# Performance work log

Measured on AMD Instinct MI355X. Metric: run time of the kernel, lower is better.

## Reference

```python
import jax, jax.numpy as jnp
import numpy as np

N_NODES = 50000
N_EDGES = 800000
IN_CH = 128
HID = 32
HEADS = 4
LATENT = 64
NEG_SLOPE = 0.2  # PyG GATConv default


def setup_inputs() -> dict:
    key = jax.random.key(0)
    ks = jax.random.split(key, 12)
    HC = HID * HEADS
    inp = {
        "x": jax.random.normal(ks[0], (N_NODES, IN_CH), dtype=jnp.float32),
        "edge_index": jax.random.randint(ks[1], (2, N_EDGES), 0, N_NODES, dtype=jnp.int64),
        # GATConv params
        "W_gat": jax.random.normal(ks[2], (IN_CH, HC), dtype=jnp.float32) / np.sqrt(IN_CH),
        "b_gat": jnp.zeros((HC,), dtype=jnp.float32),
        "att_src": jax.random.normal(ks[3], (HEADS, HID), dtype=jnp.float32) / np.sqrt(HID),
        "att_dst": jax.random.normal(ks[4], (HEADS, HID), dtype=jnp.float32) / np.sqrt(HID),
        # encoder / decoder / output linears
        "W_enc": jax.random.normal(ks[5], (HC, LATENT), dtype=jnp.float32) / np.sqrt(HC),
        "b_enc": jnp.zeros((LATENT,), dtype=jnp.float32),
        "W_dec": jax.random.normal(ks[6], (LATENT, HC), dtype=jnp.float32) / np.sqrt(LATENT),
        "b_dec": jnp.zeros((HC,), dtype=jnp.float32),
        "W_out": jax.random.normal(ks[7], (HC, IN_CH), dtype=jnp.float32) / np.sqrt(HC),
        "b_out": jnp.zeros((IN_CH,), dtype=jnp.float32),
    }
    return inp


def reference(x, edge_index, W_gat, b_gat, att_src, att_dst,
              W_enc, b_enc, W_dec, b_dec, W_out, b_out):
    N = x.shape[0]
    H, C = att_src.shape
    # PyG GATConv adds self-loops by default
    loops = jnp.arange(N, dtype=edge_index.dtype)
    src = jnp.concatenate([edge_index[0], loops])  # message sources (x_j)
    dst = jnp.concatenate([edge_index[1], loops])  # aggregation targets (x_i)

    h = (x @ W_gat).reshape(N, H, C)               # [N,H,C]
    a_src = jnp.einsum('nhc,hc->nh', h, att_src)   # [N,H]
    a_dst = jnp.einsum('nhc,hc->nh', h, att_dst)   # [N,H]

    e = jax.nn.leaky_relu(a_src[src] + a_dst[dst], NEG_SLOPE)  # [E,H]
    # segment softmax over destination nodes (numerically stable)
    e_max = jax.ops.segment_max(e, dst, num_segments=N)
    e_exp = jnp.exp(e - e_max[dst])
    denom = jax.ops.segment_sum(e_exp, dst, num_segments=N)
    alpha = e_exp / (denom[dst] + 1e-16)           # [E,H]

    msg = h[src] * alpha[:, :, None]               # [E,H,C]
    agg = jax.ops.segment_sum(msg, dst, num_segments=N)  # [N,H,C]
    gat_out = agg.reshape(N, H * C) + b_gat        # concat heads + bias

    x1 = jax.nn.elu(gat_out)
    encoded = x1 @ W_enc + b_enc
    decoded = encoded @ W_dec + b_dec
    x2 = jax.nn.elu(decoded)
    return x2 @ W_out + b_out
```

## Files before the change

### kernel.cpp

```cpp
#include <hip/hip_runtime.h>
#include <hip/hip_bf16.h>

#define N_NODES 50000
#define N_EDGES 800000
#define BM 64
#define NBUCK 196
#define CAP 8192
#define CHUNK 2048
#define NB_BUCKET_BLOCKS ((N_EDGES + CHUNK - 1) / CHUNK)
#define SWZ_BLOCKS 192
#define SWZ_G 32768
#define BFT 1024
#define GBLK ((N_NODES + BM - 1) / BM)

typedef _Float16 half4v __attribute__((ext_vector_type(4)));
typedef _Float16 half8 __attribute__((ext_vector_type(8)));
typedef float    float4v __attribute__((ext_vector_type(4)));

__device__ __forceinline__ float elu_f(float v) {
    return (v > 0.f) ? v : (__expf(v) - 1.f);
}

__device__ __forceinline__ unsigned f2bf2(float a, float b) {
    unsigned ua = __float_as_uint(a), ub = __float_as_uint(b);
    ua = (ua + 0x7FFFu + ((ua >> 16) & 1u)) >> 16;
    ub = (ub + 0x7FFFu + ((ub >> 16) & 1u)) >> 16;
    return ua | (ub << 16);
}
__device__ __forceinline__ float2 bf2f2(unsigned u) {
    float2 f;
    f.x = __uint_as_float(u << 16);
    f.y = __uint_as_float(u & 0xFFFF0000u);
    return f;
}

__global__ __launch_bounds__(256) void k_pre(const void* __restrict__ e_raw,
        int* __restrict__ flag,
        const float* __restrict__ We, const float* __restrict__ Wd,
        const float* __restrict__ Wo, const float* __restrict__ Wg,
        _Float16* __restrict__ swz, int* __restrict__ bcursor) {
    const int b = blockIdx.x;
    const int tid = threadIdx.x;
    if (b >= SWZ_BLOCKS) {
        __shared__ int nz;
        if (tid == 0) nz = 0;
        bcursor[tid] = 0;
        __syncthreads();
        int cnt = 0;
        const unsigned* er = (const unsigned*)e_raw;
        for (int i = tid; i < 2048; i += 256)
            if (er[2 * i + 1] != 0u) cnt = 1;
        if (cnt) atomicOr(&nz, 1);
        __syncthreads();
        if (tid == 0) *flag = (nz == 0) ? 1 : 0;
        return;
    }
    int t = b * 256 + tid;
    const float* W; int base, N;
    if (t < 8192)       { W = We; base = 0;     N = 64;  }
    else if (t < 16384) { W = Wd; base = 8192;  N = 128; }
    else if (t < 32768) { W = Wo; base = 16384; N = 128; }
    else                { W = Wg; base = SWZ_G; N = 128; }
    int loc = t - base;
    int nnt = N >> 4;
    int frag = loc >> 9, r = loc & 511, lane = r >> 3, j = r & 7;
    int kc = frag / nnt, nt = frag - kc * nnt;
    int k = kc * 32 + ((lane >> 4) << 3) + j;
    int n = nt * 16 + (lane & 15);
    swz[t] = (_Float16)W[k * N + n];
}

__global__ __launch_bounds__(256) void k_gatlin_bucket(
        const float* __restrict__ x, const _Float16* __restrict__ swz,
        const float* __restrict__ att_s, const float* __restrict__ att_d,
        unsigned* __restrict__ h_bf, float* __restrict__ a_src,
        float* __restrict__ a_dst,
        const void* __restrict__ e_raw, const int* __restrict__ flag,
        int* __restrict__ bcursor, uint2* __restrict__ ebuck) {
    __shared__ __align__(16) char smem[50176];
    const int tid = threadIdx.x;

    if (blockIdx.x < NB_BUCKET_BLOCKS) {
        int* lh    = (int*)smem;
        int* gbase = (int*)(smem + 1024);
        int* lcur  = (int*)(smem + 2048);
        const int base = blockIdx.x * CHUNK;
        const int is64 = *flag;
        const long long* e64 = (const long long*)e_raw;
        const int* e32 = (const int*)e_raw;

        lh[tid] = 0;
        __syncthreads();
#pragma unroll 4
        for (int j = 0; j < CHUNK / 256; j++) {
            int e = base + j * 256 + tid;
            if (e < N_EDGES) {
                int d = is64 ? (int)e64[N_EDGES + e] : e32[N_EDGES + e];
                atomicAdd(&lh[d >> 8], 1);
            }
        }
        __syncthreads();
        if (lh[tid]) gbase[tid] = atomicAdd(&bcursor[tid], lh[tid]);
        lcur[tid] = 0;
        __syncthreads();
#pragma unroll 4
        for (int j = 0; j < CHUNK / 256; j++) {
            int e = base + j * 256 + tid;
            if (e < N_EDGES) {
                int sN, d;
                if (is64) { sN = (int)e64[e]; d = (int)e64[N_EDGES + e]; }
                else      { sN = e32[e];      d = e32[N_EDGES + e]; }
                int bb = d >> 8;
                int idx = gbase[bb] + atomicAdd(&lcur[bb], 1);
                if (idx < CAP) {
                    uint2 pr; pr.x = (unsigned)sN; pr.y = (unsigned)d;
                    ebuck[bb * CAP + idx] = pr;
                }
            }
        }
        return;
    }

    _Float16* sx = (_Float16*)smem;
    float*    sh = (float*)(smem + 16384);
    const int m0 = (blockIdx.x - NB_BUCKET_BLOCKS) * 64;

#pragma unroll
    for (int i = 0; i < 8; i++) {
        int idx = tid + i * 256;
        int r = idx >> 5, c4 = idx & 31;
        int row = m0 + r; if (row >= N_NODES) row = N_NODES - 1;
        float4 v = ((const float4*)(x + (size_t)row * 128))[c4];
        half4v h;
        h[0] = (_Float16)v.x; h[1] = (_Float16)v.y;
        h[2] = (_Float16)v.z; h[3] = (_Float16)v.w;
        *(half4v*)&sx[r * 128 + c4 * 4] = h;
    }
    __syncthreads();

    const int wave = tid >> 6, lane = tid & 63;
    const int lm = lane & 15, lq = lane >> 4;
    const int wrow = wave * 16;

    {
        float4v acc[8];
#pragma unroll
        for (int nt = 0; nt < 8; nt++) acc[nt] = (float4v){0.f, 0.f, 0.f, 0.f};
#pragma unroll
        for (int kc = 0; kc < 4; kc++) {
            half8 a = *(const half8*)&sx[(wrow + lm) * 128 + kc * 32 + lq * 8];
#pragma unroll
            for (int nt = 0; nt < 8; nt++) {
                half8 b = *(const half8*)&swz[SWZ_G + (kc * 8 + nt) * 512 + lane * 8];
                acc[nt] = __builtin_amdgcn_mfma_f32_16x16x32_f16(a, b, acc[nt], 0, 0, 0);
            }
        }
#pragma unroll
        for (int nt = 0; nt < 8; nt++)
#pragma unroll
            for (int r = 0; r < 4; r++)
                sh[(wrow + lq * 4 + r) * 132 + nt * 16 + lm] = acc[nt][r];
    }
    __syncthreads();

    const int c0 = (tid & 31) * 4;
    const int r0 = (tid >> 5) * 8;
    float4 as4 = *(const float4*)&att_s[c0];
    float4 ad4 = *(const float4*)&att_d[c0];
    const int head = c0 >> 5;

#pragma unroll
    for (int r = 0; r < 8; r++) {
        int row = m0 + r0 + r;
        bool ok = row < N_NODES;
        float4 hv = *(const float4*)&sh[(r0 + r) * 132 + c0];
        if (ok) {
            uint2 p;
            p.x = f2bf2(hv.x, hv.y);
            p.y = f2bf2(hv.z, hv.w);
            *(uint2*)&h_bf[(size_t)row * 64 + (c0 >> 1)] = p;
        }
        float vs = hv.x * as4.x + hv.y * as4.y + hv.z * as4.z + hv.w * as4.w;
        float vd = hv.x * ad4.x + hv.y * ad4.y + hv.z * ad4.z + hv.w * ad4.w;
#pragma unroll
        for (int o = 4; o >= 1; o >>= 1) {
            vs += __shfl_down(vs, o, 8);
            vd += __shfl_down(vd, o, 8);
        }
        if (ok && (tid & 7) == 0) {
            a_src[row * 4 + head] = vs;
            a_dst[row * 4 + head] = vd;
        }
    }
}

__global__ __launch_bounds__(BFT) void k_bfill(const uint2* __restrict__ ebuck,
        const int* __restrict__ bcursor, int2* __restrict__ nodeoff,
        int* __restrict__ csr_src) {
    __shared__ int lh[256];
    __shared__ int lexc[256];
    __shared__ int lcur[256];
    const int tid = threadIdx.x;
    const int b = blockIdx.x;
    const int lo = b * CAP;
    int cnt = bcursor[b]; if (cnt > CAP) cnt = CAP;
    const int hi = lo + cnt;
    const int n0 = b << 8;

    if (tid < 256) { lh[tid] = 0; lcur[tid] = 0; }
    __syncthreads();
    for (int i = lo + tid; i < hi; i += BFT)
        atomicAdd(&lh[ebuck[i].y & 255], 1);
    __syncthreads();

    int v = 0, p = 0;
    if (tid < 256) {
        v = lh[tid];
        p = (v + 7) & ~7;
        lexc[tid] = p;
    }
    __syncthreads();
    for (int o = 1; o < 256; o <<= 1) {
        int u = (tid < 256 && tid >= o) ? lexc[tid - o] : 0;
        __syncthreads();
        if (tid < 256) lexc[tid] += u;
        __syncthreads();
    }
    if (tid < 256) {
        int s = lexc[tid] - p;
        lexc[tid] = s;
        int node = n0 + tid;
        if (node < N_NODES) {
            int2 no;
            no.x = lo + s;
            int maxlen = CAP - s; if (maxlen < 0) maxlen = 0;
            no.y = p <= maxlen ? p : (maxlen & ~7);
            nodeoff[node] = no;
        }
    }
    __syncthreads();

    for (int i = lo + tid; i < hi; i += BFT) {
        uint2 pr = ebuck[i];
        int li = (int)(pr.y & 255);
        int pos = atomicAdd(&lcur[li], 1);
        int dst = lexc[li] + pos;
        if (dst < CAP) csr_src[lo + dst] = (int)pr.x;
    }
    if (tid < 256) {
        int base = lexc[tid];
        for (int j = v; j < p && base + j < CAP; j++) csr_src[lo + base + j] = -1;
    }
}

__global__ __launch_bounds__(256) void k_gather(const int2* __restrict__ nodeoff,
        const int* __restrict__ csr_src, const float* __restrict__ a_src,
        const float* __restrict__ a_dst, const unsigned* __restrict__ h_bf,
        float* __restrict__ agg) {
    int d = blockIdx.x * 4 + (threadIdx.x >> 6);
    if (d >= N_NODES) return;
    const int lane = threadIdx.x & 63;
    const int half = lane >> 5;
    const int l32 = lane & 31;
    const int hd = l32 >> 3;
    int2 nd = nodeoff[d];
    const int lo = nd.x, hi = nd.x + nd.y;

    const float adh = a_dst[d * 4 + hd];

    float den = 0.f;
    float ax = 0.f, ay = 0.f, az = 0.f, aw = 0.f;

    if (half == 0) {
        float t = a_src[d * 4 + hd] + adh;
        t = t > 0.f ? t : 0.2f * t;
        float es = __expf(t);
        den = es;
        uint2 hu = ((const uint2*)(h_bf + (size_t)d * 64))[l32];
        float2 c01 = bf2f2(hu.x), c23 = bf2f2(hu.y);
        ax = c01.x * es; ay = c01.y * es;
        az = c23.x * es; aw = c23.y * es;
    }

    for (int base = lo; base < hi; base += 8) {
        int i0 = base + half;
        int s0 = csr_src[i0 + 0];
        int s1 = csr_src[i0 + 2];
        int s2 = csr_src[i0 + 4];
        int s3 = csr_src[i0 + 6];
        int g0 = s0 < 0 ? d : s0;
        int g1 = s1 < 0 ? d : s1;
        int g2 = s2 < 0 ? d : s2;
        int g3 = s3 < 0 ? d : s3;
        uint2 u0 = ((const uint2*)(h_bf + (size_t)g0 * 64))[l32];
        uint2 u1 = ((const uint2*)(h_bf + (size_t)g1 * 64))[l32];
        uint2 u2 = ((const uint2*)(h_bf + (size_t)g2 * 64))[l32];
        uint2 u3 = ((const uint2*)(h_bf + (size_t)g3 * 64))[l32];
        float a0 = a_src[g0 * 4 + hd];
        float a1 = a_src[g1 * 4 + hd];
        float a2 = a_src[g2 * 4 + hd];
        float a3 = a_src[g3 * 4 + hd];

        float t0 = a0 + adh; t0 = t0 > 0.f ? t0 : 0.2f * t0;
        float t1 = a1 + adh; t1 = t1 > 0.f ? t1 : 0.2f * t1;
        float t2 = a2 + adh; t2 = t2 > 0.f ? t2 : 0.2f * t2;
        float t3 = a3 + adh; t3 = t3 > 0.f ? t3 : 0.2f * t3;
        float e0 = s0 < 0 ? 0.f : __expf(t0);
        float e1 = s1 < 0 ? 0.f : __expf(t1);
        float e2 = s2 < 0 ? 0.f : __expf(t2);
        float e3 = s3 < 0 ? 0.f : __expf(t3);
        den += (e0 + e1) + (e2 + e3);

        float2 p, q;
        p = bf2f2(u0.x); q = bf2f2(u0.y);
        ax = fmaf(p.x, e0, ax); ay = fmaf(p.y, e0, ay);
        az = fmaf(q.x, e0, az); aw = fmaf(q.y, e0, aw);
        p = bf2f2(u1.x); q = bf2f2(u1.y);
        ax = fmaf(p.x, e1, ax); ay = fmaf(p.y, e1, ay);
        az = fmaf(q.x, e1, az); aw = fmaf(q.y, e1, aw);
        p = bf2f2(u2.x); q = bf2f2(u2.y);
        ax = fmaf(p.x, e2, ax); ay = fmaf(p.y, e2, ay);
        az = fmaf(q.x, e2, az); aw = fmaf(q.y, e2, aw);
        p = bf2f2(u3.x); q = bf2f2(u3.y);
        ax = fmaf(p.x, e3, ax); ay = fmaf(p.y, e3, ay);
        az = fmaf(q.x, e3, az); aw = fmaf(q.y, e3, aw);
    }

    den += __shfl_xor(den, 32);
    ax += __shfl_xor(ax, 32);
    ay += __shfl_xor(ay, 32);
    az += __shfl_xor(az, 32);
    aw += __shfl_xor(aw, 32);

    if (half == 0) {
        float inv = 1.f / (den + 1e-16f);
        float4 o; o.x = ax * inv; o.y = ay * inv; o.z = az * inv; o.w = aw * inv;
        ((float4*)(agg + (size_t)d * 128))[l32] = o;
    }
}

__global__ __launch_bounds__(256) void k_mlp(const float* __restrict__ agg,
        const float* __restrict__ b_gat, const _Float16* __restrict__ swz,
        const float* __restrict__ b_enc, const float* __restrict__ b_dec,
        const float* __restrict__ b_out, float* __restrict__ out) {
    __shared__ _Float16 sx[64 * 128];
    __shared__ _Float16 se[4 * 16 * 64];
    const int tid = threadIdx.x;
    const int m0 = blockIdx.x * 64;

#pragma unroll
    for (int i = 0; i < 8; i++) {
        int idx = tid + i * 256;
        int r = idx >> 5, c4 = idx & 31;
        int row = m0 + r; if (row >= N_NODES) row = N_NODES - 1;
        float4 v = ((const float4*)(agg + (size_t)row * 128))[c4];
        float4 bg = ((const float4*)b_gat)[c4];
        half4v h;
        h[0] = (_Float16)elu_f(v.x + bg.x);
        h[1] = (_Float16)elu_f(v.y + bg.y);
        h[2] = (_Float16)elu_f(v.z + bg.z);
        h[3] = (_Float16)elu_f(v.w + bg.w);
        *(half4v*)&sx[r * 128 + c4 * 4] = h;
    }
    __syncthreads();

    const int wave = tid >> 6, lane = tid & 63;
    const int lm = lane & 15, lq = lane >> 4;
    const int wrow = wave * 16;
    _Float16* eslab = &se[wave * 16 * 64];

    {
        float4v acc[4];
#pragma unroll
        for (int nt = 0; nt < 4; nt++) acc[nt] = (float4v){0.f, 0.f, 0.f, 0.f};
#pragma unroll
        for (int kc = 0; kc < 4; kc++) {
            half8 a = *(const half8*)&sx[(wrow + lm) * 128 + kc * 32 + lq * 8];
#pragma unroll
            for (int nt = 0; nt < 4; nt++) {
                half8 b = *(const half8*)&swz[(kc * 4 + nt) * 512 + lane * 8];
                acc[nt] = __builtin_amdgcn_mfma_f32_16x16x32_f16(a, b, acc[nt], 0, 0, 0);
            }
        }
#pragma unroll
        for (int nt = 0; nt < 4; nt++) {
            float be = b_enc[nt * 16 + lm];
#pragma unroll
            for (int r = 0; r < 4; r++)
                eslab[(lq * 4 + r) * 64 + nt * 16 + lm] = (_Float16)(acc[nt][r] + be);
        }
    }

    {
        float4v acc[8];
#pragma unroll
        for (int nt = 0; nt < 8; nt++) acc[nt] = (float4v){0.f, 0.f, 0.f, 0.f};
#pragma unroll
        for (int kc = 0; kc < 2; kc++) {
            half8 a = *(const half8*)&eslab[lm * 64 + kc * 32 + lq * 8];
#pragma unroll
            for (int nt = 0; nt < 8; nt++) {
                half8 b = *(const half8*)&swz[8192 + (kc * 8 + nt) * 512 + lane * 8];
                acc[nt] = __builtin_amdgcn_mfma_f32_16x16x32_f16(a, b, acc[nt], 0, 0, 0);
            }
        }
#pragma unroll
        for (int nt = 0; nt < 8; nt++) {
            float bd = b_dec[nt * 16 + lm];
#pragma unroll
            for (int r = 0; r < 4; r++)
                sx[(wrow + lq * 4 + r) * 128 + nt * 16 + lm] =
                    (_Float16)elu_f(acc[nt][r] + bd);
        }
    }

    {
        float4v acc[8];
#pragma unroll
        for (int nt = 0; nt < 8; nt++) acc[nt] = (float4v){0.f, 0.f, 0.f, 0.f};
#pragma unroll
        for (int kc = 0; kc < 4; kc++) {
            half8 a = *(const half8*)&sx[(wrow + lm) * 128 + kc * 32 + lq * 8];
#pragma unroll
            for (int nt = 0; nt < 8; nt++) {
                half8 b = *(const half8*)&swz[16384 + (kc * 8 + nt) * 512 + lane * 8];
                acc[nt] = __builtin_amdgcn_mfma_f32_16x16x32_f16(a, b, acc[nt], 0, 0, 0);
            }
        }
#pragma unroll
        for (int nt = 0; nt < 8; nt++) {
            float bo = b_out[nt * 16 + lm];
#pragma unroll
            for (int r = 0; r < 4; r++) {
                int row = m0 + wrow + lq * 4 + r;
                if (row < N_NODES)
                    out[(size_t)row * 128 + nt * 16 + lm] = acc[nt][r] + bo;
            }
        }
    }
}

extern "C" void kernel_launch(void* const* d_in, const int* in_sizes, int n_in,
                              void* d_out, int out_size, void* d_ws, size_t ws_size,
                              hipStream_t stream) {
    const float* x       = (const float*)d_in[0];
    const void*  e_raw   = d_in[1];
    const float* W_gat   = (const float*)d_in[2];
    const float* b_gat   = (const float*)d_in[3];
    const float* att_src = (const float*)d_in[4];
    const float* att_dst = (const float*)d_in[5];
    const float* W_enc   = (const float*)d_in[6];
    const float* b_enc   = (const float*)d_in[7];
    const float* W_dec   = (const float*)d_in[8];
    const float* b_dec   = (const float*)d_in[9];
    const float* W_out   = (const float*)d_in[10];
    const float* b_out   = (const float*)d_in[11];
    float* out = (float*)d_out;

    float* ws      = (float*)d_ws;
    float*   hreg  = ws;
    unsigned* h_bf = (unsigned*)hreg;
    float* a_src   = hreg + 6400000;
    float* a_dst   = a_src + 200000;
    float* agg     = a_dst + 200000;
    uint2* ebuck   = (uint2*)agg;
    int*   csr_src = (int*)(agg + 6400000);
    int2*  nodeoff = (int2*)(csr_src + NBUCK * CAP);
    int*   flag    = (int*)(nodeoff + 50000);
    int*   bcursor = flag + 1;
    _Float16* swz  = (_Float16*)(((uintptr_t)(bcursor + 256) + 15) & ~(uintptr_t)15);

    k_pre<<<SWZ_BLOCKS + 1, 256, 0, stream>>>(
        e_raw, flag, W_enc, W_dec, W_out, W_gat, swz, bcursor);

    k_gatlin_bucket<<<NB_BUCKET_BLOCKS + GBLK, 256, 0, stream>>>(
        x, swz, att_src, att_dst, h_bf, a_src, a_dst,
        e_raw, flag, bcursor, ebuck);

    k_bfill<<<NBUCK, BFT, 0, stream>>>(ebuck, bcursor, nodeoff, csr_src);

    k_gather<<<(N_NODES + 3) / 4, 256, 0, stream>>>(nodeoff, csr_src, a_src, a_dst, h_bf, agg);

    k_mlp<<<GBLK, 256, 0, stream>>>(agg, b_gat, swz, b_enc, b_dec, b_out, out);
}
```

Measured before the change: 187.4 us.

## Fuse GAT gather with MLP kernel, keep aggregated rows in shared memory

Merges the edge-gather/softmax aggregation kernel with the three-layer MLP kernel. Each 1024-thread block aggregates 64 nodes (4 per wave) directly into an fp16 shared tile with bias and ELU applied, then runs the MFMA layers with the 16 waves split across row and column tiles. This removes the fp32 agg write and read round trip through global memory, plus one kernel launch. In exchange it adds block-wide barriers between the MLP stages, and the larger blocks may lower occupancy or scheduling flexibility for the latency-bound gather.

```diff
diff --git a/kernel.cpp b/kernel.cpp
--- a/kernel.cpp
+++ b/kernel.cpp
@@ -253,188 +253,178 @@
     }
 }
 
-__global__ __launch_bounds__(256) void k_gather(const int2* __restrict__ nodeoff,
-        const int* __restrict__ csr_src, const float* __restrict__ a_src,
-        const float* __restrict__ a_dst, const unsigned* __restrict__ h_bf,
-        float* __restrict__ agg) {
-    int d = blockIdx.x * 4 + (threadIdx.x >> 6);
-    if (d >= N_NODES) return;
-    const int lane = threadIdx.x & 63;
+__global__ __launch_bounds__(1024) void k_gather_mlp(
+        const int2* __restrict__ nodeoff, const int* __restrict__ csr_src,
+        const float* __restrict__ a_src, const float* __restrict__ a_dst,
+        const unsigned* __restrict__ h_bf, const float* __restrict__ b_gat,
+        const _Float16* __restrict__ swz, const float* __restrict__ b_enc,
+        const float* __restrict__ b_dec, const float* __restrict__ b_out,
+        float* __restrict__ out) {
+    __shared__ _Float16 sx[64 * 128];
+    __shared__ _Float16 se[64 * 64];
+    const int tid = threadIdx.x;
+    const int wave = tid >> 6, lane = tid & 63;
+    const int m0 = blockIdx.x * 64;
     const int half = lane >> 5;
     const int l32 = lane & 31;
     const int hd = l32 >> 3;
-    int2 nd = nodeoff[d];
-    const int lo = nd.x, hi = nd.x + nd.y;
-
-    const float adh = a_dst[d * 4 + hd];
-
-    float den = 0.f;
-    float ax = 0.f, ay = 0.f, az = 0.f, aw = 0.f;
-
-    if (half == 0) {
-        float t = a_src[d * 4 + hd] + adh;
-        t = t > 0.f ? t : 0.2f * t;
-        float es = __expf(t);
-        den = es;
-        uint2 hu = ((const uint2*)(h_bf + (size_t)d * 64))[l32];
-        float2 c01 = bf2f2(hu.x), c23 = bf2f2(hu.y);
-        ax = c01.x * es; ay = c01.y * es;
-        az = c23.x * es; aw = c23.y * es;
-    }
-
-    for (int base = lo; base < hi; base += 8) {
-        int i0 = base + half;
-        int s0 = csr_src[i0 + 0];
-        int s1 = csr_src[i0 + 2];
-        int s2 = csr_src[i0 + 4];
-        int s3 = csr_src[i0 + 6];
-        int g0 = s0 < 0 ? d : s0;
-        int g1 = s1 < 0 ? d : s1;
-        int g2 = s2 < 0 ? d : s2;
-        int g3 = s3 < 0 ? d : s3;
-        uint2 u0 = ((const uint2*)(h_bf + (size_t)g0 * 64))[l32];
-        uint2 u1 = ((const uint2*)(h_bf + (size_t)g1 * 64))[l32];
-        uint2 u2 = ((const uint2*)(h_bf + (size_t)g2 * 64))[l32];
-        uint2 u3 = ((const uint2*)(h_bf + (size_t)g3 * 64))[l32];
-        float a0 = a_src[g0 * 4 + hd];
-        float a1 = a_src[g1 * 4 + hd];
-        float a2 = a_src[g2 * 4 + hd];
-        float a3 = a_src[g3 * 4 + hd];
-
-        float t0 = a0 + adh; t0 = t0 > 0.f ? t0 : 0.2f * t0;
-        float t1 = a1 + adh; t1 = t1 > 0.f ? t1 : 0.2f * t1;
-        float t2 = a2 + adh; t2 = t2 > 0.f ? t2 : 0.2f * t2;
-        float t3 = a3 + adh; t3 = t3 > 0.f ? t3 : 0.2f * t3;
-        float e0 = s0 < 0 ? 0.f : __expf(t0);
-        float e1 = s1 < 0 ? 0.f : __expf(t1);
-        float e2 = s2 < 0 ? 0.f : __expf(t2);
-        float e3 = s3 < 0 ? 0.f : __expf(t3);
-        den += (e0 + e1) + (e2 + e3);
-
-        float2 p, q;
-        p = bf2f2(u0.x); q = bf2f2(u0.y);
-        ax = fmaf(p.x, e0, ax); ay = fmaf(p.y, e0, ay);
-        az = fmaf(q.x, e0, az); aw = fmaf(q.y, e0, aw);
-        p = bf2f2(u1.x); q = bf2f2(u1.y);
-        ax = fmaf(p.x, e1, ax); ay = fmaf(p.y, e1, ay);
-        az = fmaf(q.x, e1, az); aw = fmaf(q.y, e1, aw);
-        p = bf2f2(u2.x); q = bf2f2(u2.y);
-        ax = fmaf(p.x, e2, ax); ay = fmaf(p.y, e2, ay);
-        az = fmaf(q.x, e2, az); aw = fmaf(q.y, e2, aw);
-        p = bf2f2(u3.x); q = bf2f2(u3.y);
-        ax = fmaf(p.x, e3, ax); ay = fmaf(p.y, e3, ay);
-        az = fmaf(q.x, e3, az); aw = fmaf(q.y, e3, aw);
-    }
-
-    den += __shfl_xor(den, 32);
-    ax += __shfl_xor(ax, 32);
-    ay += __shfl_xor(ay, 32);
-    az += __shfl_xor(az, 32);
-    aw += __shfl_xor(aw, 32);
-
-    if (half == 0) {
-        float inv = 1.f / (den + 1e-16f);
-        float4 o; o.x = ax * inv; o.y = ay * inv; o.z = az * inv; o.w = aw * inv;
-        ((float4*)(agg + (size_t)d * 128))[l32] = o;
-    }
-}
-
-__global__ __launch_bounds__(256) void k_mlp(const float* __restrict__ agg,
-        const float* __restrict__ b_gat, const _Float16* __restrict__ swz,
-        const float* __restrict__ b_enc, const float* __restrict__ b_dec,
-        const float* __restrict__ b_out, float* __restrict__ out) {
-    __shared__ _Float16 sx[64 * 128];
-    __shared__ _Float16 se[4 * 16 * 64];
-    const int tid = threadIdx.x;
-    const int m0 = blockIdx.x * 64;
-
-#pragma unroll
-    for (int i = 0; i < 8; i++) {
-        int idx = tid + i * 256;
-        int r = idx >> 5, c4 = idx & 31;
-        int row = m0 + r; if (row >= N_NODES) row = N_NODES - 1;
-        float4 v = ((const float4*)(agg + (size_t)row * 128))[c4];
-        float4 bg = ((const float4*)b_gat)[c4];
-        half4v h;
-        h[0] = (_Float16)elu_f(v.x + bg.x);
-        h[1] = (_Float16)elu_f(v.y + bg.y);
-        h[2] = (_Float16)elu_f(v.z + bg.z);
-        h[3] = (_Float16)elu_f(v.w + bg.w);
-        *(half4v*)&sx[r * 128 + c4 * 4] = h;
-    }
-    __syncthreads();
-
-    const int wave = tid >> 6, lane = tid & 63;
+    const float4 bg = ((const float4*)b_gat)[l32];
+
+    for (int k = 0; k < 4; k++) {
+        const int r = wave * 4 + k;
+        const int d = m0 + r;
+        if (d < N_NODES) {
+            int2 nd = nodeoff[d];
+            const int lo = nd.x, hi = nd.x + nd.y;
+            const float adh = a_dst[d * 4 + hd];
+
+            float den = 0.f;
+            float ax = 0.f, ay = 0.f, az = 0.f, aw = 0.f;
+
+            if (half == 0) {
+                float t = a_src[d * 4 + hd] + adh;
+                t = t > 0.f ? t : 0.2f * t;
+                float es = __expf(t);
+                den = es;
+                uint2 hu = ((const uint2*)(h_bf + (size_t)d * 64))[l32];
+                float2 c01 = bf2f2(hu.x), c23 = bf2f2(hu.y);
+                ax = c01.x * es; ay = c01.y * es;
+                az = c23.x * es; aw = c23.y * es;
+            }
+
+            for (int base = lo; base < hi; base += 8) {
+                int i0 = base + half;
+                int s0 = csr_src[i0 + 0];
+                int s1 = csr_src[i0 + 2];
+                int s2 = csr_src[i0 + 4];
+                int s3 = csr_src[i0 + 6];
+                int g0 = s0 < 0 ? d : s0;
+                int g1 = s1 < 0 ? d : s1;
+                int g2 = s2 < 0 ? d : s2;
+                int g3 = s3 < 0 ? d : s3;
+                uint2 u0 = ((const uint2*)(h_bf + (size_t)g0 * 64))[l32];
+                uint2 u1 = ((const uint2*)(h_bf + (size_t)g1 * 64))[l32];
+                uint2 u2 = ((const uint2*)(h_bf + (size_t)g2 * 64))[l32];
+                uint2 u3 = ((const uint2*)(h_bf + (size_t)g3 * 64))[l32];
+                float a0 = a_src[g0 * 4 + hd];
+                float a1 = a_src[g1 * 4 + hd];
+                float a2 = a_src[g2 * 4 + hd];
+                float a3 = a_src[g3 * 4 + hd];
+
+                float t0 = a0 + adh; t0 = t0 > 0.f ? t0 : 0.2f * t0;
+                float t1 = a1 + adh; t1 = t1 > 0.f ? t1 : 0.2f * t1;
+                float t2 = a2 + adh; t2 = t2 > 0.f ? t2 : 0.2f * t2;
+                float t3 = a3 + adh; t3 = t3 > 0.f ? t3 : 0.2f * t3;
+                float e0 = s0 < 0 ? 0.f : __expf(t0);
+                float e1 = s1 < 0 ? 0.f : __expf(t1);
+                float e2 = s2 < 0 ? 0.f : __expf(t2);
+                float e3 = s3 < 0 ? 0.f : __expf(t3);
+                den += (e0 + e1) + (e2 + e3);
+
+                float2 p, q;
+                p = bf2f2(u0.x); q = bf2f2(u0.y);
+                ax = fmaf(p.x, e0, ax); ay = fmaf(p.y, e0, ay);
+                az = fmaf(q.x, e0, az); aw = fmaf(q.y, e0, aw);
+                p = bf2f2(u1.x); q = bf2f2(u1.y);
+                ax = fmaf(p.x, e1, ax); ay = fmaf(p.y, e1, ay);
+                az = fmaf(q.x, e1, az); aw = fmaf(q.y, e1, aw);
+                p = bf2f2(u2.x); q = bf2f2(u2.y);
+                ax = fmaf(p.x, e2, ax); ay = fmaf(p.y, e2, ay);
+                az = fmaf(q.x, e2, az); aw = fmaf(q.y, e2, aw);
+                p = bf2f2(u3.x); q = bf2f2(u3.y);
+                ax = fmaf(p.x, e3, ax); ay = fmaf(p.y, e3, ay);
+                az = fmaf(q.x, e3, az); aw = fmaf(q.y, e3, aw);
+            }
+
+            den += __shfl_xor(den, 32);
+            ax += __shfl_xor(ax, 32);
+            ay += __shfl_xor(ay, 32);
+            az += __shfl_xor(az, 32);
+            aw += __shfl_xor(aw, 32);
+
+            if (half == 0) {
+                float inv = 1.f / (den + 1e-16f);
+                half4v h4;
+                h4[0] = (_Float16)elu_f(fmaf(ax, inv, bg.x));
+                h4[1] = (_Float16)elu_f(fmaf(ay, inv, bg.y));
+                h4[2] = (_Float16)elu_f(fmaf(az, inv, bg.z));
+                h4[3] = (_Float16)elu_f(fmaf(aw, inv, bg.w));
+                *(half4v*)&sx[r * 128 + l32 * 4] = h4;
+            }
+        } else if (half == 0) {
+            *(half4v*)&sx[r * 128 + l32 * 4] = (half4v){0, 0, 0, 0};
+        }
+    }
+    __syncthreads();
+
     const int lm = lane & 15, lq = lane >> 4;
-    const int wrow = wave * 16;
-    _Float16* eslab = &se[wave * 16 * 64];
+    const int wr = wave >> 2, wn = wave & 3;
+    const int wrow = wr * 16;
 
     {
-        float4v acc[4];
-#pragma unroll
-        for (int nt = 0; nt < 4; nt++) acc[nt] = (float4v){0.f, 0.f, 0.f, 0.f};
+        float4v acc = (float4v){0.f, 0.f, 0.f, 0.f};
 #pragma unroll
         for (int kc = 0; kc < 4; kc++) {
             half8 a = *(const half8*)&sx[(wrow + lm) * 128 + kc * 32 + lq * 8];
-#pragma unroll
-            for (int nt = 0; nt < 4; nt++) {
-                half8 b = *(const half8*)&swz[(kc * 4 + nt) * 512 + lane * 8];
-                acc[nt] = __builtin_amdgcn_mfma_f32_16x16x32_f16(a, b, acc[nt], 0, 0, 0);
-            }
-        }
-#pragma unroll
-        for (int nt = 0; nt < 4; nt++) {
-            float be = b_enc[nt * 16 + lm];
-#pragma unroll
-            for (int r = 0; r < 4; r++)
-                eslab[(lq * 4 + r) * 64 + nt * 16 + lm] = (_Float16)(acc[nt][r] + be);
-        }
-    }
+            half8 b = *(const half8*)&swz[(kc * 4 + wn) * 512 + lane * 8];
+            acc = __builtin_amdgcn_mfma_f32_16x16x32_f16(a, b, acc, 0, 0, 0);
+        }
+        float be = b_enc[wn * 16 + lm];
+#pragma unroll
+        for (int r = 0; r < 4; r++)
+            se[(wrow + lq * 4 + r) * 64 + wn * 16 + lm] = (_Float16)(acc[r] + be);
+    }
+    __syncthreads();
 
     {
-        float4v acc[8];
-#pragma unroll
-        for (int nt = 0; nt < 8; nt++) acc[nt] = (float4v){0.f, 0.f, 0.f, 0.f};
+        float4v acc[2];
+        acc[0] = (float4v){0.f, 0.f, 0.f, 0.f};
+        acc[1] = (float4v){0.f, 0.f, 0.f, 0.f};
 #pragma unroll
         for (int kc = 0; kc < 2; kc++) {
-            half8 a = *(const half8*)&eslab[lm * 64 + kc * 32 + lq * 8];
-#pragma unroll
-            for (int nt = 0; nt < 8; nt++) {
+            half8 a = *(const half8*)&se[(wrow + lm) * 64 + kc * 32 + lq * 8];
+#pragma unroll
+            for (int t = 0; t < 2; t++) {
+                int nt = wn * 2 + t;
                 half8 b = *(const half8*)&swz[8192 + (kc * 8 + nt) * 512 + lane * 8];
-                acc[nt] = __builtin_amdgcn_mfma_f32_16x16x32_f16(a, b, acc[nt], 0, 0, 0);
-            }
-        }
-#pragma unroll
-        for (int nt = 0; nt < 8; nt++) {
+                acc[t] = __builtin_amdgcn_mfma_f32_16x16x32_f16(a, b, acc[t], 0, 0, 0);
+            }
+        }
+#pragma unroll
+        for (int t = 0; t < 2; t++) {
+            int nt = wn * 2 + t;
             float bd = b_dec[nt * 16 + lm];
 #pragma unroll
             for (int r = 0; r < 4; r++)
                 sx[(wrow + lq * 4 + r) * 128 + nt * 16 + lm] =
-                    (_Float16)elu_f(acc[nt][r] + bd);
-        }
-    }
+                    (_Float16)elu_f(acc[t][r] + bd);
+        }
+    }
+    __syncthreads();
 
     {
-        float4v acc[8];
-#pragma unroll
-        for (int nt = 0; nt < 8; nt++) acc[nt] = (float4v){0.f, 0.f, 0.f, 0.f};
+        float4v acc[2];
+        acc[0] = (float4v){0.f, 0.f, 0.f, 0.f};
+        acc[1] = (float4v){0.f, 0.f, 0.f, 0.f};
 #pragma unroll
         for (int kc = 0; kc < 4; kc++) {
             half8 a = *(const half8*)&sx[(wrow + lm) * 128 + kc * 32 + lq * 8];
 #pragma unroll
-            for (int nt = 0; nt < 8; nt++) {
+            for (int t = 0; t < 2; t++) {
+                int nt = wn * 2 + t;
                 half8 b = *(const half8*)&swz[16384 + (kc * 8 + nt) * 512 + lane * 8];
-                acc[nt] = __builtin_amdgcn_mfma_f32_16x16x32_f16(a, b, acc[nt], 0, 0, 0);
-            }
-        }
-#pragma unroll
-        for (int nt = 0; nt < 8; nt++) {
+                acc[t] = __builtin_amdgcn_mfma_f32_16x16x32_f16(a, b, acc[t], 0, 0, 0);
+            }
+        }
+#pragma unroll
+        for (int t = 0; t < 2; t++) {
+            int nt = wn * 2 + t;
             float bo = b_out[nt * 16 + lm];
 #pragma unroll
             for (int r = 0; r < 4; r++) {
                 int row = m0 + wrow + lq * 4 + r;
                 if (row < N_NODES)
-                    out[(size_t)row * 128 + nt * 16 + lm] = acc[nt][r] + bo;
+                    out[(size_t)row * 128 + nt * 16 + lm] = acc[t][r] + bo;
             }
         }
     }
@@ -479,7 +469,7 @@
 
     k_bfill<<<NBUCK, BFT, 0, stream>>>(ebuck, bcursor, nodeoff, csr_src);
 
-    k_gather<<<(N_NODES + 3) / 4, 256, 0, stream>>>(nodeoff, csr_src, a_src, a_dst, h_bf, agg);
-
-    k_mlp<<<GBLK, 256, 0, stream>>>(agg, b_gat, swz, b_enc, b_dec, b_out, out);
-}
+    k_gather_mlp<<<GBLK, 1024, 0, stream>>>(
+        nodeoff, csr_src, a_src, a_dst, h_bf, b_gat, swz,
+        b_enc, b_dec, b_out, out);
+}
```

Result: no change. 190.6 us (+1.7%).

## Fuse bias+ELU into gather, store fp16 activations, pad LDS rows

Applied to the files above, without the earlier changes.

The gather kernel now applies the GAT bias and ELU and writes fp16 x1 instead of fp32 agg, which halves the intermediate write and read between gather and MLP. The MLP kernel just copies fp16 rows into shared memory. Shared-memory row strides are padded (136 and 72 halves) to reduce LDS bank conflicts on the MFMA operand loads. Index arithmetic in gather moves to 32-bit unsigned to trim address computation. Rounding to fp16 happens slightly earlier than before, but the MLP already converted to fp16, so precision is effectively unchanged.

```diff
diff --git a/kernel.cpp b/kernel.cpp
--- a/kernel.cpp
+++ b/kernel.cpp
@@ -12,6 +12,8 @@
 #define SWZ_G 32768
 #define BFT 1024
 #define GBLK ((N_NODES + BM - 1) / BM)
+#define SXP 136
+#define SEP 72
 
 typedef _Float16 half4v __attribute__((ext_vector_type(4)));
 typedef _Float16 half8 __attribute__((ext_vector_type(8)));
@@ -77,7 +79,7 @@
         float* __restrict__ a_dst,
         const void* __restrict__ e_raw, const int* __restrict__ flag,
         int* __restrict__ bcursor, uint2* __restrict__ ebuck) {
-    __shared__ __align__(16) char smem[50176];
+    __shared__ __align__(16) char smem[64 * SXP * 2 + 64 * 132 * 4];
     const int tid = threadIdx.x;
 
     if (blockIdx.x < NB_BUCKET_BLOCKS) {
@@ -122,7 +124,7 @@
     }
 
     _Float16* sx = (_Float16*)smem;
-    float*    sh = (float*)(smem + 16384);
+    float*    sh = (float*)(smem + 64 * SXP * 2);
     const int m0 = (blockIdx.x - NB_BUCKET_BLOCKS) * 64;
 
 #pragma unroll
@@ -134,7 +136,7 @@
         half4v h;
         h[0] = (_Float16)v.x; h[1] = (_Float16)v.y;
         h[2] = (_Float16)v.z; h[3] = (_Float16)v.w;
-        *(half4v*)&sx[r * 128 + c4 * 4] = h;
+        *(half4v*)&sx[r * SXP + c4 * 4] = h;
     }
     __syncthreads();
 
@@ -148,7 +150,7 @@
         for (int nt = 0; nt < 8; nt++) acc[nt] = (float4v){0.f, 0.f, 0.f, 0.f};
 #pragma unroll
         for (int kc = 0; kc < 4; kc++) {
-            half8 a = *(const half8*)&sx[(wrow + lm) * 128 + kc * 32 + lq * 8];
+            half8 a = *(const half8*)&sx[(wrow + lm) * SXP + kc * 32 + lq * 8];
 #pragma unroll
             for (int nt = 0; nt < 8; nt++) {
                 half8 b = *(const half8*)&swz[SWZ_G + (kc * 8 + nt) * 512 + lane * 8];
@@ -256,27 +258,28 @@
 __global__ __launch_bounds__(256) void k_gather(const int2* __restrict__ nodeoff,
         const int* __restrict__ csr_src, const float* __restrict__ a_src,
         const float* __restrict__ a_dst, const unsigned* __restrict__ h_bf,
-        float* __restrict__ agg) {
+        const float* __restrict__ b_gat, _Float16* __restrict__ x1) {
     int d = blockIdx.x * 4 + (threadIdx.x >> 6);
     if (d >= N_NODES) return;
     const int lane = threadIdx.x & 63;
     const int half = lane >> 5;
     const int l32 = lane & 31;
     const int hd = l32 >> 3;
+    const uint2* hb = (const uint2*)h_bf;
     int2 nd = nodeoff[d];
     const int lo = nd.x, hi = nd.x + nd.y;
 
-    const float adh = a_dst[d * 4 + hd];
+    const float adh = a_dst[(unsigned)(d * 4 + hd)];
 
     float den = 0.f;
     float ax = 0.f, ay = 0.f, az = 0.f, aw = 0.f;
 
     if (half == 0) {
-        float t = a_src[d * 4 + hd] + adh;
+        float t = a_src[(unsigned)(d * 4 + hd)] + adh;
         t = t > 0.f ? t : 0.2f * t;
         float es = __expf(t);
         den = es;
-        uint2 hu = ((const uint2*)(h_bf + (size_t)d * 64))[l32];
+        uint2 hu = hb[(unsigned)(d << 5) + l32];
         float2 c01 = bf2f2(hu.x), c23 = bf2f2(hu.y);
         ax = c01.x * es; ay = c01.y * es;
         az = c23.x * es; aw = c23.y * es;
@@ -288,14 +291,14 @@
         int s1 = csr_src[i0 + 2];
         int s2 = csr_src[i0 + 4];
         int s3 = csr_src[i0 + 6];
-        int g0 = s0 < 0 ? d : s0;
-        int g1 = s1 < 0 ? d : s1;
-        int g2 = s2 < 0 ? d : s2;
-        int g3 = s3 < 0 ? d : s3;
-        uint2 u0 = ((const uint2*)(h_bf + (size_t)g0 * 64))[l32];
-        uint2 u1 = ((const uint2*)(h_bf + (size_t)g1 * 64))[l32];
-        uint2 u2 = ((const uint2*)(h_bf + (size_t)g2 * 64))[l32];
-        uint2 u3 = ((const uint2*)(h_bf + (size_t)g3 * 64))[l32];
+        unsigned g0 = (unsigned)(s0 < 0 ? d : s0);
+        unsigned g1 = (unsigned)(s1 < 0 ? d : s1);
+        unsigned g2 = (unsigned)(s2 < 0 ? d : s2);
+        unsigned g3 = (unsigned)(s3 < 0 ? d : s3);
+        uint2 u0 = hb[(g0 << 5) + l32];
+        uint2 u1 = hb[(g1 << 5) + l32];
+        uint2 u2 = hb[(g2 << 5) + l32];
+        uint2 u3 = hb[(g3 << 5) + l32];
         float a0 = a_src[g0 * 4 + hd];
         float a1 = a_src[g1 * 4 + hd];
         float a2 = a_src[g2 * 4 + hd];
@@ -334,40 +337,39 @@
 
     if (half == 0) {
         float inv = 1.f / (den + 1e-16f);
-        float4 o; o.x = ax * inv; o.y = ay * inv; o.z = az * inv; o.w = aw * inv;
-        ((float4*)(agg + (size_t)d * 128))[l32] = o;
-    }
-}
-
-__global__ __launch_bounds__(256) void k_mlp(const float* __restrict__ agg,
-        const float* __restrict__ b_gat, const _Float16* __restrict__ swz,
-        const float* __restrict__ b_enc, const float* __restrict__ b_dec,
-        const float* __restrict__ b_out, float* __restrict__ out) {
-    __shared__ _Float16 sx[64 * 128];
-    __shared__ _Float16 se[4 * 16 * 64];
+        float4 bg = ((const float4*)b_gat)[l32];
+        half4v h4;
+        h4[0] = (_Float16)elu_f(fmaf(ax, inv, bg.x));
+        h4[1] = (_Float16)elu_f(fmaf(ay, inv, bg.y));
+        h4[2] = (_Float16)elu_f(fmaf(az, inv, bg.z));
+        h4[3] = (_Float16)elu_f(fmaf(aw, inv, bg.w));
+        *(half4v*)&x1[(size_t)d * 128 + l32 * 4] = h4;
+    }
+}
+
+__global__ __launch_bounds__(256) void k_mlp(const _Float16* __restrict__ x1,
+        const _Float16* __restrict__ swz, const float* __restrict__ b_enc,
+        const float* __restrict__ b_dec, const float* __restrict__ b_out,
+        float* __restrict__ out) {
+    __shared__ _Float16 sx[64 * SXP];
+    __shared__ _Float16 se[4 * 16 * SEP];
     const int tid = threadIdx.x;
     const int m0 = blockIdx.x * 64;
 
 #pragma unroll
-    for (int i = 0; i < 8; i++) {
+    for (int i = 0; i < 4; i++) {
         int idx = tid + i * 256;
-        int r = idx >> 5, c4 = idx & 31;
+        int r = idx >> 4, c = idx & 15;
         int row = m0 + r; if (row >= N_NODES) row = N_NODES - 1;
-        float4 v = ((const float4*)(agg + (size_t)row * 128))[c4];
-        float4 bg = ((const float4*)b_gat)[c4];
-        half4v h;
-        h[0] = (_Float16)elu_f(v.x + bg.x);
-        h[1] = (_Float16)elu_f(v.y + bg.y);
-        h[2] = (_Float16)elu_f(v.z + bg.z);
-        h[3] = (_Float16)elu_f(v.w + bg.w);
-        *(half4v*)&sx[r * 128 + c4 * 4] = h;
+        uint4 v = ((const uint4*)(x1 + (size_t)row * 128))[c];
+        *(uint4*)&sx[r * SXP + c * 8] = v;
     }
     __syncthreads();
 
     const int wave = tid >> 6, lane = tid & 63;
     const int lm = lane & 15, lq = lane >> 4;
     const int wrow = wave * 16;
-    _Float16* eslab = &se[wave * 16 * 64];
+    _Float16* eslab = &se[wave * 16 * SEP];
 
     {
         float4v acc[4];
@@ -375,7 +377,7 @@
         for (int nt = 0; nt < 4; nt++) acc[nt] = (float4v){0.f, 0.f, 0.f, 0.f};
 #pragma unroll
         for (int kc = 0; kc < 4; kc++) {
-            half8 a = *(const half8*)&sx[(wrow + lm) * 128 + kc * 32 + lq * 8];
+            half8 a = *(const half8*)&sx[(wrow + lm) * SXP + kc * 32 + lq * 8];
 #pragma unroll
             for (int nt = 0; nt < 4; nt++) {
                 half8 b = *(const half8*)&swz[(kc * 4 + nt) * 512 + lane * 8];
@@ -387,7 +389,7 @@
             float be = b_enc[nt * 16 + lm];
 #pragma unroll
             for (int r = 0; r < 4; r++)
-                eslab[(lq * 4 + r) * 64 + nt * 16 + lm] = (_Float16)(acc[nt][r] + be);
+                eslab[(lq * 4 + r) * SEP + nt * 16 + lm] = (_Float16)(acc[nt][r] + be);
         }
     }
 
@@ -397,7 +399,7 @@
         for (int nt = 0; nt < 8; nt++) acc[nt] = (float4v){0.f, 0.f, 0.f, 0.f};
 #pragma unroll
         for (int kc = 0; kc < 2; kc++) {
-            half8 a = *(const half8*)&eslab[lm * 64 + kc * 32 + lq * 8];
+            half8 a = *(const half8*)&eslab[lm * SEP + kc * 32 + lq * 8];
 #pragma unroll
             for (int nt = 0; nt < 8; nt++) {
                 half8 b = *(const half8*)&swz[8192 + (kc * 8 + nt) * 512 + lane * 8];
@@ -409,7 +411,7 @@
             float bd = b_dec[nt * 16 + lm];
 #pragma unroll
             for (int r = 0; r < 4; r++)
-                sx[(wrow + lq * 4 + r) * 128 + nt * 16 + lm] =
+                sx[(wrow + lq * 4 + r) * SXP + nt * 16 + lm] =
                     (_Float16)elu_f(acc[nt][r] + bd);
         }
     }
@@ -420,7 +422,7 @@
         for (int nt = 0; nt < 8; nt++) acc[nt] = (float4v){0.f, 0.f, 0.f, 0.f};
 #pragma unroll
         for (int kc = 0; kc < 4; kc++) {
-            half8 a = *(const half8*)&sx[(wrow + lm) * 128 + kc * 32 + lq * 8];
+            half8 a = *(const half8*)&sx[(wrow + lm) * SXP + kc * 32 + lq * 8];
 #pragma unroll
             for (int nt = 0; nt < 8; nt++) {
                 half8 b = *(const half8*)&swz[16384 + (kc * 8 + nt) * 512 + lane * 8];
@@ -464,6 +466,7 @@
     float* a_dst   = a_src + 200000;
     float* agg     = a_dst + 200000;
     uint2* ebuck   = (uint2*)agg;
+    _Float16* x1   = (_Float16*)agg;
     int*   csr_src = (int*)(agg + 6400000);
     int2*  nodeoff = (int2*)(csr_src + NBUCK * CAP);
     int*   flag    = (int*)(nodeoff + 50000);
@@ -479,7 +482,8 @@
 
     k_bfill<<<NBUCK, BFT, 0, stream>>>(ebuck, bcursor, nodeoff, csr_src);
 
-    k_gather<<<(N_NODES + 3) / 4, 256, 0, stream>>>(nodeoff, csr_src, a_src, a_dst, h_bf, agg);
-
-    k_mlp<<<GBLK, 256, 0, stream>>>(agg, b_gat, swz, b_enc, b_dec, b_out, out);
-}
+    k_gather<<<(N_NODES + 3) / 4, 256, 0, stream>>>(
+        nodeoff, csr_src, a_src, a_dst, h_bf, b_gat, x1);
+
+    k_mlp<<<GBLK, 256, 0, stream>>>(x1, swz, b_enc, b_dec, b_out, out);
+}
```

Measured after the change: 186.3 us. Within noise of the previous version (-0.6%).
